# Kernel optimization log

Measured on AMD Instinct MI355X. Metric: run time of the kernel, lower is better.

Reference implementation:

```python
import jax, jax.numpy as jnp
import numpy as np

B, C, H, W = 16, 4, 64, 64
D_MODEL, D_INNER, D_STATE, D_CONV, DT_RANK = 64, 128, 16, 4, 4


def _mamba_params(key, prefix):
    ks = jax.random.split(key, 6)
    s = lambda k, shape, scale: jax.random.normal(k, shape, jnp.float32) * scale
    return {
        prefix + 'in_proj_w': s(ks[0], (2 * D_INNER, D_MODEL), 0.05),
        prefix + 'conv_w': s(ks[1], (D_INNER, 1, D_CONV), 0.2),
        prefix + 'conv_b': jnp.zeros((D_INNER,), jnp.float32),
        prefix + 'x_proj_w': s(ks[2], (DT_RANK + 2 * D_STATE, D_INNER), 0.05),
        prefix + 'dt_proj_w': s(ks[3], (D_INNER, DT_RANK), 0.1),
        prefix + 'dt_proj_b': s(ks[4], (D_INNER,), 0.1),
        prefix + 'A_log': jnp.log(jnp.broadcast_to(jnp.arange(1, D_STATE + 1, dtype=jnp.float32), (D_INNER, D_STATE))),
        prefix + 'D': jnp.ones((D_INNER,), jnp.float32),
        prefix + 'out_proj_w': s(ks[5], (D_MODEL, D_INNER), 0.05),
    }


def setup_inputs() -> dict:
    key = jax.random.key(0)
    ks = jax.random.split(key, 5)
    inp = {'z_damaged': jax.random.normal(ks[0], (B, C, H, W), jnp.float32)}
    inp['emb_w'] = jax.random.normal(ks[1], (D_MODEL, C), jnp.float32) * 0.1
    inp['emb_b'] = jnp.zeros((D_MODEL,), jnp.float32)
    inp.update(_mamba_params(ks[2], 'm1_'))
    inp.update(_mamba_params(ks[3], 'm2_'))
    inp['ln1_g'] = jnp.ones((D_MODEL,), jnp.float32)
    inp['ln1_b'] = jnp.zeros((D_MODEL,), jnp.float32)
    inp['ln2_g'] = jnp.ones((D_MODEL,), jnp.float32)
    inp['ln2_b'] = jnp.zeros((D_MODEL,), jnp.float32)
    inp['head_w'] = jax.random.normal(ks[4], (C, D_MODEL), jnp.float32) * 0.1
    inp['head_b'] = jnp.zeros((C,), jnp.float32)
    return inp


def _silu(x):
    return x * jax.nn.sigmoid(x)


def _layernorm(x, g, b, eps=1e-5):
    mu = x.mean(-1, keepdims=True)
    var = ((x - mu) ** 2).mean(-1, keepdims=True)
    return (x - mu) * jax.lax.rsqrt(var + eps) * g + b


def _mamba(x, in_proj_w, conv_w, conv_b, x_proj_w, dt_proj_w, dt_proj_b, A_log, Dp, out_proj_w):
    Bb, L, _ = x.shape
    xz = x @ in_proj_w.T                      # [B,L,2*Di]
    u, z = jnp.split(xz, 2, axis=-1)
    # causal depthwise conv over the sequence axis (left-pad K-1)
    uc = jnp.transpose(u, (0, 2, 1))          # [B,Di,L]
    uc = jax.lax.conv_general_dilated(uc, conv_w, (1,), [(D_CONV - 1, 0)],
                                      dimension_numbers=('NCH', 'OIH', 'NCH'),
                                      feature_group_count=D_INNER)
    uc = uc + conv_b[None, :, None]
    u = _silu(jnp.transpose(uc, (0, 2, 1)))   # [B,L,Di]
    x_dbl = u @ x_proj_w.T                    # [B,L,dt_rank+2N]
    dt, Bm, Cm = jnp.split(x_dbl, [DT_RANK, DT_RANK + D_STATE], axis=-1)
    dt = jax.nn.softplus(dt @ dt_proj_w.T + dt_proj_b)   # [B,L,Di]
    A = -jnp.exp(A_log)                       # [Di,N]
    dA = jnp.exp(jnp.einsum('bld,dn->bldn', dt, A))      # [B,L,Di,N]
    dBu = jnp.einsum('bld,bln,bld->bldn', dt, Bm, u)     # [B,L,Di,N]

    def step(h, inp):
        dA_t, dBu_t, C_t = inp
        h = dA_t * h + dBu_t                  # [B,Di,N]
        return h, jnp.einsum('bdn,bn->bd', h, C_t)

    h0 = jnp.zeros((Bb, D_INNER, D_STATE), x.dtype)
    _, ys = jax.lax.scan(step, h0, (jnp.moveaxis(dA, 1, 0), jnp.moveaxis(dBu, 1, 0), jnp.moveaxis(Cm, 1, 0)))
    y = jnp.moveaxis(ys, 0, 1) + u * Dp       # [B,L,Di]
    y = y * _silu(z)
    return y @ out_proj_w.T                   # [B,L,D_MODEL]


def reference(z_damaged, emb_w, emb_b,
              m1_in_proj_w, m1_conv_w, m1_conv_b, m1_x_proj_w, m1_dt_proj_w, m1_dt_proj_b, m1_A_log, m1_D, m1_out_proj_w,
              m2_in_proj_w, m2_conv_w, m2_conv_b, m2_x_proj_w, m2_dt_proj_w, m2_dt_proj_b, m2_A_log, m2_D, m2_out_proj_w,
              ln1_g, ln1_b, ln2_g, ln2_b, head_w, head_b):
    Bz, Cz, Hh, Ww = z_damaged.shape
    zf = jnp.transpose(z_damaged, (0, 2, 3, 1)).reshape(Bz, Hh * Ww, Cz)
    feat = zf @ emb_w.T + emb_b
    feat = _mamba(feat, m1_in_proj_w, m1_conv_w, m1_conv_b, m1_x_proj_w, m1_dt_proj_w, m1_dt_proj_b, m1_A_log, m1_D, m1_out_proj_w)
    feat = _layernorm(feat, ln1_g, ln1_b)
    feat = _mamba(feat, m2_in_proj_w, m2_conv_w, m2_conv_b, m2_x_proj_w, m2_dt_proj_w, m2_dt_proj_b, m2_A_log, m2_D, m2_out_proj_w)
    feat = _layernorm(feat, ln2_g, ln2_b)
    drift = feat @ head_w.T + head_b          # [B,L,C]
    drift = jnp.transpose(drift.reshape(Bz, Hh, Ww, Cz), (0, 3, 1, 2))
    return z_damaged - drift
```

## Files before the change

kernel.cpp:

```cpp
#include <hip/hip_runtime.h>
#include <hip/hip_bf16.h>

#define DEV __device__ __forceinline__

static constexpr int Bn = 16;
static constexpr int Cc = 4;
static constexpr int HW = 4096;
static constexpr int BL = Bn * HW;
static constexpr int DM = 64;
static constexpr int DI = 128;
static constexpr int NS = 16;
static constexpr int NC = 256;
static constexpr int CS = HW / NC;

DEV float sigmoid_f(float x) { return 1.f / (1.f + __expf(-x)); }
DEV float softplus_f(float x) {
    return fmaxf(x, 0.f) + __logf(1.f + __expf(-fabsf(x)));
}
DEV float silu_f(float x) { return x / (1.f + __expf(-x)); }

__global__ __launch_bounds__(256) void k_embed(const float* __restrict__ z,
                                               const float* __restrict__ ew,
                                               const float* __restrict__ eb,
                                               float* __restrict__ feat) {
    int idx = blockIdx.x * 256 + threadIdx.x;
    if (idx >= BL * DM) return;
    int m = idx & 63;
    int bl = idx >> 6;
    int b = bl >> 12;
    int hw = bl & 4095;
    const float* zp = z + (size_t)b * Cc * HW + hw;
    float acc = eb[m];
#pragma unroll
    for (int c = 0; c < 4; ++c) acc += zp[(size_t)c * HW] * ew[m * 4 + c];
    feat[idx] = acc;
}

__global__ __launch_bounds__(256) void k_ln(float* __restrict__ feat,
                                            const float* __restrict__ g,
                                            const float* __restrict__ bta, int R) {
    int lane = threadIdx.x & 63;
    int wv = blockIdx.x * 4 + (threadIdx.x >> 6);
    int stride = gridDim.x * 4;
    for (int row = wv; row < R; row += stride) {
        float x = feat[(size_t)row * 64 + lane];
        float s = x;
#pragma unroll
        for (int off = 32; off; off >>= 1) s += __shfl_xor(s, off, 64);
        float mu = s * (1.f / 64.f);
        float xm = x - mu;
        float v = xm * xm;
#pragma unroll
        for (int off = 32; off; off >>= 1) v += __shfl_xor(v, off, 64);
        float var = v * (1.f / 64.f);
        feat[(size_t)row * 64 + lane] = xm * rsqrtf(var + 1e-5f) * g[lane] + bta[lane];
    }
}

template <int K, int BN>
__global__ __launch_bounds__(256) void k_gemm(const float* __restrict__ in,
                                              const float* __restrict__ W,
                                              float* __restrict__ out,
                                              int Nfull) {
    constexpr int BM = 64, TM = 4, TN = 4;
    constexpr int CT = BN / TN;
    constexpr int RT = BM / TM;
    constexpr int KP = K + 4;
    constexpr int WP = BN + 4;
    __shared__ float As[BM * KP];
    __shared__ float Ws[K * WP];
    int tid = threadIdx.x;
    int n0 = blockIdx.y * BN;
    int row0 = blockIdx.x * BM;
    for (int i = tid; i < BN * (K / 4); i += 256) {
        int k4 = i / BN;
        int c = i - k4 * BN;
        float4 w = *reinterpret_cast<const float4*>(&W[(size_t)(n0 + c) * K + k4 * 4]);
        Ws[(k4 * 4 + 0) * WP + c] = w.x;
        Ws[(k4 * 4 + 1) * WP + c] = w.y;
        Ws[(k4 * 4 + 2) * WP + c] = w.z;
        Ws[(k4 * 4 + 3) * WP + c] = w.w;
    }
    for (int i = tid; i < BM * (K / 4); i += 256) {
        int r = i / (K / 4);
        int k4 = i - r * (K / 4);
        *reinterpret_cast<float4*>(&As[r * KP + k4 * 4]) =
            *reinterpret_cast<const float4*>(&in[(size_t)(row0 + r) * K + k4 * 4]);
    }
    __syncthreads();
    int ty = tid / CT, tx = tid - (tid / CT) * CT;
    int c0 = tx * TN;
    float acc[TM][TN];
#pragma unroll
    for (int i = 0; i < TM; ++i)
#pragma unroll
        for (int c = 0; c < TN; ++c) acc[i][c] = 0.f;
#pragma unroll 4
    for (int k = 0; k < K; k += 4) {
        float4 a[TM];
#pragma unroll
        for (int i = 0; i < TM; ++i)
            a[i] = *reinterpret_cast<const float4*>(&As[(ty + i * RT) * KP + k]);
        float4 b0 = *reinterpret_cast<const float4*>(&Ws[(k + 0) * WP + c0]);
        float4 b1 = *reinterpret_cast<const float4*>(&Ws[(k + 1) * WP + c0]);
        float4 b2 = *reinterpret_cast<const float4*>(&Ws[(k + 2) * WP + c0]);
        float4 b3 = *reinterpret_cast<const float4*>(&Ws[(k + 3) * WP + c0]);
#pragma unroll
        for (int i = 0; i < TM; ++i) {
            acc[i][0] += a[i].x * b0.x + a[i].y * b1.x + a[i].z * b2.x + a[i].w * b3.x;
            acc[i][1] += a[i].x * b0.y + a[i].y * b1.y + a[i].z * b2.y + a[i].w * b3.y;
            acc[i][2] += a[i].x * b0.z + a[i].y * b1.z + a[i].z * b2.z + a[i].w * b3.z;
            acc[i][3] += a[i].x * b0.w + a[i].y * b1.w + a[i].z * b2.w + a[i].w * b3.w;
        }
    }
#pragma unroll
    for (int i = 0; i < TM; ++i) {
        size_t o = (size_t)(row0 + ty + i * RT) * Nfull + n0 + c0;
        float4 v = {acc[i][0], acc[i][1], acc[i][2], acc[i][3]};
        *reinterpret_cast<float4*>(&out[o]) = v;
    }
}

__global__ __launch_bounds__(256) void k_xproj(const float* __restrict__ xz,
                                               const float* __restrict__ W,
                                               const float* __restrict__ cw,
                                               const float* __restrict__ cb,
                                               float* __restrict__ xdbl) {
    constexpr int BM = 64, K = 128, BN = 36, TN = 3, TM = 4;
    constexpr int CT = BN / TN;
    constexpr int RT = BM / TM;
    constexpr int KP = K + 4;
    constexpr int WP = BN + 4;
    __shared__ float Xs[(BM + 3) * KP];
    __shared__ float Ws[K * WP];
    int tid = threadIdx.x;
    int row0 = blockIdx.x * BM;
    bool first = (row0 & 4095) == 0;
    for (int i = tid; i < BN * (K / 4); i += 256) {
        int k4 = i / BN;
        int c = i - k4 * BN;
        float4 w = *reinterpret_cast<const float4*>(&W[(size_t)c * K + k4 * 4]);
        Ws[(k4 * 4 + 0) * WP + c] = w.x;
        Ws[(k4 * 4 + 1) * WP + c] = w.y;
        Ws[(k4 * 4 + 2) * WP + c] = w.z;
        Ws[(k4 * 4 + 3) * WP + c] = w.w;
    }
    for (int i = tid; i < (BM + 3) * (K / 4); i += 256) {
        int r = i / (K / 4);
        int k4 = i - r * (K / 4);
        float4 v = {0, 0, 0, 0};
        if (!first || r >= 3)
            v = *reinterpret_cast<const float4*>(&xz[(size_t)(row0 - 3 + r) * 256 + k4 * 4]);
        *reinterpret_cast<float4*>(&Xs[r * KP + k4 * 4]) = v;
    }
    __syncthreads();
    {
        int rg = tid >> 5;
        int c0 = (tid & 31) * 4;
        float4 wr[4];
#pragma unroll
        for (int j = 0; j < 4; ++j)
            wr[j] = *reinterpret_cast<const float4*>(&cw[(c0 + j) * 4]);
        float4 cb4 = *reinterpret_cast<const float4*>(&cb[c0]);
        int R0 = rg * 8;
        float4 xr[11];
#pragma unroll
        for (int j = 0; j < 11; ++j)
            xr[j] = *reinterpret_cast<const float4*>(&Xs[(R0 + j) * KP + c0]);
        float4 ur[8];
#pragma unroll
        for (int j = 0; j < 8; ++j) {
            float4 acc;
            acc.x = cb4.x + wr[0].x * xr[j].x + wr[0].y * xr[j + 1].x + wr[0].z * xr[j + 2].x + wr[0].w * xr[j + 3].x;
            acc.y = cb4.y + wr[1].x * xr[j].y + wr[1].y * xr[j + 1].y + wr[1].z * xr[j + 2].y + wr[1].w * xr[j + 3].y;
            acc.z = cb4.z + wr[2].x * xr[j].z + wr[2].y * xr[j + 1].z + wr[2].z * xr[j + 2].z + wr[2].w * xr[j + 3].z;
            acc.w = cb4.w + wr[3].x * xr[j].w + wr[3].y * xr[j + 1].w + wr[3].z * xr[j + 2].w + wr[3].w * xr[j + 3].w;
            ur[j].x = silu_f(acc.x);
            ur[j].y = silu_f(acc.y);
            ur[j].z = silu_f(acc.z);
            ur[j].w = silu_f(acc.w);
        }
        __syncthreads();
#pragma unroll
        for (int j = 0; j < 8; ++j)
            *reinterpret_cast<float4*>(&Xs[(R0 + j) * KP + c0]) = ur[j];
    }
    __syncthreads();
    if (tid < CT * RT) {
        int ty = tid / CT, tx = tid - (tid / CT) * CT;
        int c0 = tx * TN;
        float acc[TM][TN];
#pragma unroll
        for (int i = 0; i < TM; ++i)
#pragma unroll
            for (int c = 0; c < TN; ++c) acc[i][c] = 0.f;
#pragma unroll 4
        for (int k = 0; k < K; k += 4) {
            float4 a[TM];
#pragma unroll
            for (int i = 0; i < TM; ++i)
                a[i] = *reinterpret_cast<const float4*>(&Xs[(ty + i * RT) * KP + k]);
            float bv[4][TN];
#pragma unroll
            for (int j = 0; j < 4; ++j)
#pragma unroll
                for (int c = 0; c < TN; ++c) bv[j][c] = Ws[(k + j) * WP + c0 + c];
#pragma unroll
            for (int i = 0; i < TM; ++i)
#pragma unroll
                for (int c = 0; c < TN; ++c)
                    acc[i][c] += a[i].x * bv[0][c] + a[i].y * bv[1][c]
                               + a[i].z * bv[2][c] + a[i].w * bv[3][c];
        }
#pragma unroll
        for (int i = 0; i < TM; ++i) {
            size_t o = (size_t)(row0 + ty + i * RT) * BN + c0;
#pragma unroll
            for (int c = 0; c < TN; ++c) xdbl[o + c] = acc[i][c];
        }
    }
}

DEV bool load_a_struct(const float* Alog, int d, float4& a0v, float4& a1v,
                       float4& a2v, float4& a3v, float& a0) {
    const float4* al = reinterpret_cast<const float4*>(Alog + d * NS);
    float4 t0 = al[0], t1 = al[1], t2 = al[2], t3 = al[3];
    a0v.x = -__expf(t0.x); a0v.y = -__expf(t0.y); a0v.z = -__expf(t0.z); a0v.w = -__expf(t0.w);
    a1v.x = -__expf(t1.x); a1v.y = -__expf(t1.y); a1v.z = -__expf(t1.z); a1v.w = -__expf(t1.w);
    a2v.x = -__expf(t2.x); a2v.y = -__expf(t2.y); a2v.z = -__expf(t2.z); a2v.w = -__expf(t2.w);
    a3v.x = -__expf(t3.x); a3v.y = -__expf(t3.y); a3v.z = -__expf(t3.z); a3v.w = -__expf(t3.w);
    a0 = a0v.x;
    float aa[16] = {a0v.x, a0v.y, a0v.z, a0v.w, a1v.x, a1v.y, a1v.z, a1v.w,
                    a2v.x, a2v.y, a2v.z, a2v.w, a3v.x, a3v.y, a3v.z, a3v.w};
    bool fast = true;
#pragma unroll
    for (int n = 0; n < 16; ++n)
        fast = fast && (fabsf(aa[n] - a0 * (float)(n + 1)) <= 1e-4f * (float)(n + 1));
    return fast;
}

#define POWERS(dt, a0, D0, D1, D2, D3)                        \
    {                                                         \
        float E1 = __expf((dt) * (a0));                       \
        float E2 = E1 * E1, E3 = E2 * E1, E4 = E2 * E2;       \
        float E5 = E3 * E2, E6 = E3 * E3, E7 = E4 * E3;       \
        float E8 = E4 * E4, E9 = E5 * E4, E10 = E5 * E5;      \
        float E11 = E6 * E5, E12 = E6 * E6, E13 = E7 * E6;    \
        float E14 = E7 * E7, E15 = E8 * E7, E16 = E8 * E8;    \
        D0 = {E1, E2, E3, E4};                                \
        D1 = {E5, E6, E7, E8};                                \
        D2 = {E9, E10, E11, E12};                             \
        D3 = {E13, E14, E15, E16};                            \
    }

#define UPD4D(H, DA, BV)                          \
    H.x = DA.x * H.x + du * BV.x;                 \
    H.y = DA.y * H.y + du * BV.y;                 \
    H.z = DA.z * H.z + du * BV.z;                 \
    H.w = DA.w * H.w + du * BV.w;

#define UPD4E(H, A, BV)                                  \
    H.x = __expf(dt * A.x) * H.x + du * BV.x;            \
    H.y = __expf(dt * A.y) * H.y + du * BV.y;            \
    H.z = __expf(dt * A.z) * H.z + du * BV.z;            \
    H.w = __expf(dt * A.w) * H.w + du * BV.w;

#define CONV_WARMUP                                                     \
    float x3 = 0.f, x2 = 0.f, x1 = 0.f;                                 \
    if (c != 0) {                                                       \
        size_t wb = ((size_t)b * HW + t0) * 256 + d;                    \
        x3 = xz[wb - 3 * 256];                                          \
        x2 = xz[wb - 2 * 256];                                          \
        x1 = xz[wb - 1 * 256];                                          \
    }

#define CONV_STEP(base)                                                 \
    float xv = xz[(base) * 256 + d];                                    \
    float cacc = cbv + cwv.x * x3 + cwv.y * x2 + cwv.z * x1 + cwv.w * xv; \
    float uu = cacc * sigmoid_f(cacc);                                  \
    x3 = x2; x2 = x1; x1 = xv;

__global__ __launch_bounds__(128, 4) void k_scan1(const float* __restrict__ xz,
                                                  const float* __restrict__ xdbl,
                                                  const float* __restrict__ dpw,
                                                  const float* __restrict__ dpb,
                                                  const float* __restrict__ Alog,
                                                  const float* __restrict__ cw,
                                                  const float* __restrict__ cb,
                                                  float* __restrict__ cS,
                                                  float* __restrict__ cDT) {
    int blk = blockIdx.x;
    int b = blk / NC;
    int c = blk % NC;
    int d = threadIdx.x;
    float4 a0v, a1v, a2v, a3v;
    float a0;
    bool fast = load_a_struct(Alog, d, a0v, a1v, a2v, a3v, a0);
    float4 w = *reinterpret_cast<const float4*>(dpw + d * 4);
    float bb = dpb[d];
    float4 cwv = *reinterpret_cast<const float4*>(cw + d * 4);
    float cbv = cb[d];
    float4 h0 = {0, 0, 0, 0}, h1 = {0, 0, 0, 0}, h2 = {0, 0, 0, 0}, h3 = {0, 0, 0, 0};
    float sdt = 0.f;
    int t0 = c * CS;
    CONV_WARMUP
    if (fast) {
        for (int tt = 0; tt < CS; ++tt) {
            size_t base = (size_t)b * HW + t0 + tt;
            const float4* xd4 = reinterpret_cast<const float4*>(xdbl + base * 36);
            float4 x0 = xd4[0];
            float4 B0 = xd4[1], B1 = xd4[2], B2 = xd4[3], B3 = xd4[4];
            float dt = softplus_f(w.x * x0.x + w.y * x0.y + w.z * x0.z + w.w * x0.w + bb);
            CONV_STEP(base)
            float du = dt * uu;
            sdt += dt;
            float4 D0, D1, D2, D3;
            POWERS(dt, a0, D0, D1, D2, D3)
            UPD4D(h0, D0, B0) UPD4D(h1, D1, B1) UPD4D(h2, D2, B2) UPD4D(h3, D3, B3)
        }
    } else {
        for (int tt = 0; tt < CS; ++tt) {
            size_t base = (size_t)b * HW + t0 + tt;
            const float4* xd4 = reinterpret_cast<const float4*>(xdbl + base * 36);
            float4 x0 = xd4[0];
            float4 B0 = xd4[1], B1 = xd4[2], B2 = xd4[3], B3 = xd4[4];
            float dt = softplus_f(w.x * x0.x + w.y * x0.y + w.z * x0.z + w.w * x0.w + bb);
            CONV_STEP(base)
            float du = dt * uu;
            sdt += dt;
            UPD4E(h0, a0v, B0) UPD4E(h1, a1v, B1) UPD4E(h2, a2v, B2) UPD4E(h3, a3v, B3)
        }
    }
    size_t o = (size_t)blk * DI + d;
    cDT[o] = sdt;
    float4* cs4 = reinterpret_cast<float4*>(cS + o * NS);
    cs4[0] = h0; cs4[1] = h1; cs4[2] = h2; cs4[3] = h3;
}

__global__ __launch_bounds__(256) void k_scan2(float* __restrict__ cS,
                                               const float* __restrict__ cDT,
                                               const float* __restrict__ Alog) {
    int idx = blockIdx.x * 256 + threadIdx.x;
    if (idx >= Bn * DI * NS) return;
    int n = idx & 15;
    int d = (idx >> 4) & 127;
    int b = idx >> 11;
    float a = -__expf(Alog[d * NS + n]);
    float h = 0.f;
    for (int c = 0; c < NC; ++c) {
        size_t o = (size_t)(b * NC + c) * DI + d;
        float s = cS[o * NS + n];
        cS[o * NS + n] = h;
        h = __expf(a * cDT[o]) * h + s;
    }
}

__global__ __launch_bounds__(128, 4) void k_scan3(float* __restrict__ uy,
                                                  const float* __restrict__ xz,
                                                  const float* __restrict__ xdbl,
                                                  const float* __restrict__ dpw,
                                                  const float* __restrict__ dpb,
                                                  const float* __restrict__ Alog,
                                                  const float* __restrict__ Dp,
                                                  const float* __restrict__ cw,
                                                  const float* __restrict__ cb,
                                                  const float* __restrict__ iS) {
    int blk = blockIdx.x;
    int b = blk / NC;
    int c = blk % NC;
    int d = threadIdx.x;
    float4 a0v, a1v, a2v, a3v;
    float a0;
    bool fast = load_a_struct(Alog, d, a0v, a1v, a2v, a3v, a0);
    float4 w = *reinterpret_cast<const float4*>(dpw + d * 4);
    float bb = dpb[d];
    float Dv = Dp[d];
    float4 cwv = *reinterpret_cast<const float4*>(cw + d * 4);
    float cbv = cb[d];
    size_t so = (size_t)blk * DI + d;
    const float4* is4 = reinterpret_cast<const float4*>(iS + so * NS);
    float4 h0 = is4[0], h1 = is4[1], h2 = is4[2], h3 = is4[3];
    int t0 = c * CS;
    CONV_WARMUP
    if (fast) {
        for (int tt = 0; tt < CS; ++tt) {
            size_t base = (size_t)b * HW + t0 + tt;
            const float4* xd4 = reinterpret_cast<const float4*>(xdbl + base * 36);
            float4 x0 = xd4[0];
            float4 B0 = xd4[1], B1 = xd4[2], B2 = xd4[3], B3 = xd4[4];
            float4 C0 = xd4[5], C1 = xd4[6], C2 = xd4[7], C3 = xd4[8];
            float dt = softplus_f(w.x * x0.x + w.y * x0.y + w.z * x0.z + w.w * x0.w + bb);
            CONV_STEP(base)
            float du = dt * uu;
            float4 D0, D1, D2, D3;
            POWERS(dt, a0, D0, D1, D2, D3)
            UPD4D(h0, D0, B0) UPD4D(h1, D1, B1) UPD4D(h2, D2, B2) UPD4D(h3, D3, B3)
            float y = h0.x * C0.x + h0.y * C0.y + h0.z * C0.z + h0.w * C0.w
                    + h1.x * C1.x + h1.y * C1.y + h1.z * C1.z + h1.w * C1.w
                    + h2.x * C2.x + h2.y * C2.y + h2.z * C2.z + h2.w * C2.w
                    + h3.x * C3.x + h3.y * C3.y + h3.z * C3.z + h3.w * C3.w;
            y += uu * Dv;
            float zz = xz[base * 256 + 128 + d];
            y *= zz * sigmoid_f(zz);
            uy[base * DI + d] = y;
        }
    } else {
        for (int tt = 0; tt < CS; ++tt) {
            size_t base = (size_t)b * HW + t0 + tt;
            const float4* xd4 = reinterpret_cast<const float4*>(xdbl + base * 36);
            float4 x0 = xd4[0];
            float4 B0 = xd4[1], B1 = xd4[2], B2 = xd4[3], B3 = xd4[4];
            float4 C0 = xd4[5], C1 = xd4[6], C2 = xd4[7], C3 = xd4[8];
            float dt = softplus_f(w.x * x0.x + w.y * x0.y + w.z * x0.z + w.w * x0.w + bb);
            CONV_STEP(base)
            float du = dt * uu;
            UPD4E(h0, a0v, B0) UPD4E(h1, a1v, B1) UPD4E(h2, a2v, B2) UPD4E(h3, a3v, B3)
            float y = h0.x * C0.x + h0.y * C0.y + h0.z * C0.z + h0.w * C0.w
                    + h1.x * C1.x + h1.y * C1.y + h1.z * C1.z + h1.w * C1.w
                    + h2.x * C2.x + h2.y * C2.y + h2.z * C2.z + h2.w * C2.w
                    + h3.x * C3.x + h3.y * C3.y + h3.z * C3.z + h3.w * C3.w;
            y += uu * Dv;
            float zz = xz[base * 256 + 128 + d];
            y *= zz * sigmoid_f(zz);
            uy[base * DI + d] = y;
        }
    }
}

__global__ __launch_bounds__(256) void k_head(const float* __restrict__ feat,
                                              const float* __restrict__ hwt,
                                              const float* __restrict__ hb,
                                              const float* __restrict__ g,
                                              const float* __restrict__ bta,
                                              const float* __restrict__ z,
                                              float* __restrict__ out) {
    __shared__ float fl[64 * 65];
    int row0 = blockIdx.x * 64;
    for (int i = threadIdx.x; i < 64 * 64; i += 256) {
        int r = i >> 6;
        int m = i & 63;
        fl[r * 65 + m] = feat[(size_t)(row0 + r) * 64 + m];
    }
    __syncthreads();
    int r = threadIdx.x >> 2;
    int c = threadIdx.x & 3;
    int m0 = c * 16;
    float s = 0.f;
#pragma unroll
    for (int mi = 0; mi < 16; ++mi) s += fl[r * 65 + m0 + mi];
    s += __shfl_xor(s, 1, 64);
    s += __shfl_xor(s, 2, 64);
    float mu = s * (1.f / 64.f);
    float v = 0.f;
#pragma unroll
    for (int mi = 0; mi < 16; ++mi) {
        float dd = fl[r * 65 + m0 + mi] - mu;
        v += dd * dd;
    }
    v += __shfl_xor(v, 1, 64);
    v += __shfl_xor(v, 2, 64);
    float rs = rsqrtf(v * (1.f / 64.f) + 1e-5f);
#pragma unroll
    for (int mi = 0; mi < 16; ++mi) {
        int m = m0 + mi;
        float x = fl[r * 65 + m];
        fl[r * 65 + m] = (x - mu) * rs * g[m] + bta[m];
    }
    __syncthreads();
    float acc = hb[c];
#pragma unroll
    for (int m = 0; m < 64; ++m) acc += fl[r * 65 + m] * hwt[c * 64 + m];
    int bl = row0 + r;
    int b = bl >> 12;
    int hw = bl & 4095;
    size_t o = ((size_t)b * 4 + c) * HW + hw;
    out[o] = z[o] - acc;
}

static void run_mamba(const float* const* P, float* feat, float* xz, float* u,
                      float* xdbl, float* cS, float* cDT, hipStream_t s) {
    k_gemm<64, 64><<<dim3(BL / 64, 4), 256, 0, s>>>(feat, P[0], xz, 256);
    k_xproj<<<BL / 64, 256, 0, s>>>(xz, P[3], P[1], P[2], xdbl);
    k_scan1<<<Bn * NC, DI, 0, s>>>(xz, xdbl, P[4], P[5], P[6], P[1], P[2], cS, cDT);
    k_scan2<<<(Bn * DI * NS) / 256, 256, 0, s>>>(cS, cDT, P[6]);
    k_scan3<<<Bn * NC, DI, 0, s>>>(u, xz, xdbl, P[4], P[5], P[6], P[7], P[1], P[2], cS);
    k_gemm<128, 64><<<dim3(BL / 64, 1), 256, 0, s>>>(u, P[8], feat, 64);
}

extern "C" void kernel_launch(void* const* d_in, const int* in_sizes, int n_in,
                              void* d_out, int out_size, void* d_ws, size_t ws_size,
                              hipStream_t stream) {
    const float* z = (const float*)d_in[0];
    const float* ew = (const float*)d_in[1];
    const float* eb = (const float*)d_in[2];
    const float* m1[9];
    const float* m2[9];
    for (int i = 0; i < 9; ++i) m1[i] = (const float*)d_in[3 + i];
    for (int i = 0; i < 9; ++i) m2[i] = (const float*)d_in[12 + i];
    const float* ln1g = (const float*)d_in[21];
    const float* ln1b = (const float*)d_in[22];
    const float* ln2g = (const float*)d_in[23];
    const float* ln2b = (const float*)d_in[24];
    const float* hwt = (const float*)d_in[25];
    const float* hb = (const float*)d_in[26];

    float* ws = (float*)d_ws;
    float* feat = ws;
    float* xz = feat + (size_t)BL * 64;
    float* u = xz + (size_t)BL * 256;
    float* xdbl = u + (size_t)BL * 128;
    float* cS = xdbl + (size_t)BL * 36;
    float* cDT = cS + (size_t)Bn * NC * DI * NS;

    k_embed<<<(BL * DM) / 256, 256, 0, stream>>>(z, ew, eb, feat);
    run_mamba(m1, feat, xz, u, xdbl, cS, cDT, stream);
    k_ln<<<4096, 256, 0, stream>>>(feat, ln1g, ln1b, BL);
    run_mamba(m2, feat, xz, u, xdbl, cS, cDT, stream);
    k_head<<<BL / 64, 256, 0, stream>>>(feat, hwt, hb, ln2g, ln2b, z, (float*)d_out);
}
```

Before: 496.9 us.

## Replace FP32 SIMT GEMMs with bf16 MFMA matrix-core GEMMs

The in_proj and out_proj GEMMs move from a register-tiled FP32 FMA kernel to a kernel that converts inputs and weights to bf16 in shared memory and uses mfma_f32_16x16x32_bf16. The in_proj launch now covers all 256 output columns in one block instead of four column blocks, so activations are read once. The aim is to cut ALU time on the matrix ops. The cost is bf16 rounding of inputs, a risk to accuracy, plus per-block weight conversion and uncoalesced scalar output stores.

```diff
diff --git a/kernel.cpp b/kernel.cpp
--- a/kernel.cpp
+++ b/kernel.cpp
@@ -18,6 +18,15 @@
     return fmaxf(x, 0.f) + __logf(1.f + __expf(-fabsf(x)));
 }
 DEV float silu_f(float x) { return x / (1.f + __expf(-x)); }
+
+typedef short bf16x8 __attribute__((ext_vector_type(8)));
+typedef float f32x4 __attribute__((ext_vector_type(4)));
+
+DEV short f2b(float x) {
+    unsigned u = __float_as_uint(x);
+    unsigned r = (u + 0x7FFFu + ((u >> 16) & 1u)) >> 16;
+    return (short)r;
+}
 
 __global__ __launch_bounds__(256) void k_embed(const float* __restrict__ z,
                                                const float* __restrict__ ew,
@@ -57,67 +66,52 @@
     }
 }
 
-template <int K, int BN>
-__global__ __launch_bounds__(256) void k_gemm(const float* __restrict__ in,
-                                              const float* __restrict__ W,
-                                              float* __restrict__ out,
-                                              int Nfull) {
-    constexpr int BM = 64, TM = 4, TN = 4;
-    constexpr int CT = BN / TN;
-    constexpr int RT = BM / TM;
-    constexpr int KP = K + 4;
-    constexpr int WP = BN + 4;
-    __shared__ float As[BM * KP];
-    __shared__ float Ws[K * WP];
+template <int K, int NTOT>
+__global__ __launch_bounds__(256) void k_gemm_mfma(const float* __restrict__ in,
+                                                   const float* __restrict__ W,
+                                                   float* __restrict__ out) {
+    constexpr int KP = K + 8;
+    __shared__ short Wl[NTOT * KP];
+    __shared__ short Al[64 * KP];
     int tid = threadIdx.x;
-    int n0 = blockIdx.y * BN;
-    int row0 = blockIdx.x * BM;
-    for (int i = tid; i < BN * (K / 4); i += 256) {
-        int k4 = i / BN;
-        int c = i - k4 * BN;
-        float4 w = *reinterpret_cast<const float4*>(&W[(size_t)(n0 + c) * K + k4 * 4]);
-        Ws[(k4 * 4 + 0) * WP + c] = w.x;
-        Ws[(k4 * 4 + 1) * WP + c] = w.y;
-        Ws[(k4 * 4 + 2) * WP + c] = w.z;
-        Ws[(k4 * 4 + 3) * WP + c] = w.w;
-    }
-    for (int i = tid; i < BM * (K / 4); i += 256) {
+    int row0 = blockIdx.x * 64;
+    for (int i = tid; i < NTOT * (K / 4); i += 256) {
         int r = i / (K / 4);
-        int k4 = i - r * (K / 4);
-        *reinterpret_cast<float4*>(&As[r * KP + k4 * 4]) =
-            *reinterpret_cast<const float4*>(&in[(size_t)(row0 + r) * K + k4 * 4]);
+        int k4 = (i - r * (K / 4)) * 4;
+        float4 w = *reinterpret_cast<const float4*>(&W[(size_t)r * K + k4]);
+        short4 s = {f2b(w.x), f2b(w.y), f2b(w.z), f2b(w.w)};
+        *reinterpret_cast<short4*>(&Wl[r * KP + k4]) = s;
+    }
+    for (int i = tid; i < 64 * (K / 4); i += 256) {
+        int r = i / (K / 4);
+        int k4 = (i - r * (K / 4)) * 4;
+        float4 a = *reinterpret_cast<const float4*>(&in[(size_t)(row0 + r) * K + k4]);
+        short4 s = {f2b(a.x), f2b(a.y), f2b(a.z), f2b(a.w)};
+        *reinterpret_cast<short4*>(&Al[r * KP + k4]) = s;
     }
     __syncthreads();
-    int ty = tid / CT, tx = tid - (tid / CT) * CT;
-    int c0 = tx * TN;
-    float acc[TM][TN];
-#pragma unroll
-    for (int i = 0; i < TM; ++i)
-#pragma unroll
-        for (int c = 0; c < TN; ++c) acc[i][c] = 0.f;
-#pragma unroll 4
-    for (int k = 0; k < K; k += 4) {
-        float4 a[TM];
-#pragma unroll
-        for (int i = 0; i < TM; ++i)
-            a[i] = *reinterpret_cast<const float4*>(&As[(ty + i * RT) * KP + k]);
-        float4 b0 = *reinterpret_cast<const float4*>(&Ws[(k + 0) * WP + c0]);
-        float4 b1 = *reinterpret_cast<const float4*>(&Ws[(k + 1) * WP + c0]);
-        float4 b2 = *reinterpret_cast<const float4*>(&Ws[(k + 2) * WP + c0]);
-        float4 b3 = *reinterpret_cast<const float4*>(&Ws[(k + 3) * WP + c0]);
-#pragma unroll
-        for (int i = 0; i < TM; ++i) {
-            acc[i][0] += a[i].x * b0.x + a[i].y * b1.x + a[i].z * b2.x + a[i].w * b3.x;
-            acc[i][1] += a[i].x * b0.y + a[i].y * b1.y + a[i].z * b2.y + a[i].w * b3.y;
-            acc[i][2] += a[i].x * b0.z + a[i].y * b1.z + a[i].z * b2.z + a[i].w * b3.z;
-            acc[i][3] += a[i].x * b0.w + a[i].y * b1.w + a[i].z * b2.w + a[i].w * b3.w;
-        }
-    }
-#pragma unroll
-    for (int i = 0; i < TM; ++i) {
-        size_t o = (size_t)(row0 + ty + i * RT) * Nfull + n0 + c0;
-        float4 v = {acc[i][0], acc[i][1], acc[i][2], acc[i][3]};
-        *reinterpret_cast<float4*>(&out[o]) = v;
+    int w = tid >> 6;
+    int lane = tid & 63;
+    int lr = lane & 15;
+    int kh = lane >> 4;
+    int r = w * 16 + lr;
+    bf16x8 af[K / 32];
+#pragma unroll
+    for (int ka = 0; ka < K / 32; ++ka)
+        af[ka] = *reinterpret_cast<const bf16x8*>(&Al[r * KP + ka * 32 + kh * 8]);
+#pragma unroll
+    for (int ct = 0; ct < NTOT / 16; ++ct) {
+        int c = ct * 16 + lr;
+        f32x4 acc = {0.f, 0.f, 0.f, 0.f};
+#pragma unroll
+        for (int ka = 0; ka < K / 32; ++ka) {
+            bf16x8 bfr = *reinterpret_cast<const bf16x8*>(&Wl[c * KP + ka * 32 + kh * 8]);
+            acc = __builtin_amdgcn_mfma_f32_16x16x32_bf16(af[ka], bfr, acc, 0, 0, 0);
+        }
+        size_t ob = (size_t)(row0 + w * 16 + kh * 4) * NTOT + ct * 16 + lr;
+#pragma unroll
+        for (int j = 0; j < 4; ++j)
+            out[ob + (size_t)j * NTOT] = acc[j];
     }
 }
 
@@ -479,12 +473,12 @@
 
 static void run_mamba(const float* const* P, float* feat, float* xz, float* u,
                       float* xdbl, float* cS, float* cDT, hipStream_t s) {
-    k_gemm<64, 64><<<dim3(BL / 64, 4), 256, 0, s>>>(feat, P[0], xz, 256);
+    k_gemm_mfma<64, 256><<<BL / 64, 256, 0, s>>>(feat, P[0], xz);
     k_xproj<<<BL / 64, 256, 0, s>>>(xz, P[3], P[1], P[2], xdbl);
     k_scan1<<<Bn * NC, DI, 0, s>>>(xz, xdbl, P[4], P[5], P[6], P[1], P[2], cS, cDT);
     k_scan2<<<(Bn * DI * NS) / 256, 256, 0, s>>>(cS, cDT, P[6]);
     k_scan3<<<Bn * NC, DI, 0, s>>>(u, xz, xdbl, P[4], P[5], P[6], P[7], P[1], P[2], cS);
-    k_gemm<128, 64><<<dim3(BL / 64, 1), 256, 0, s>>>(u, P[8], feat, 64);
+    k_gemm_mfma<128, 64><<<BL / 64, 256, 0, s>>>(u, P[8], feat);
 }
 
 extern "C" void kernel_launch(void* const* d_in, const int* in_sizes, int n_in,
```

Result: faster. 441.0 us (-11.3%).
